# Kernel optimization log

Measured on AMD Instinct MI355X. Metric: run time of the kernel, lower is better.

The kernel has to match this reference:

```python
import jax, jax.numpy as jnp
import numpy as np

MARGIN = 0.09
SCALE_POS = 2.0
SCALE_NEG = 40.0
EPS = 1e-05
THRESH1 = 0.501
THRESH2 = 0.531


def setup_inputs() -> dict:
    key = jax.random.key(0)
    k1, k2 = jax.random.split(key)
    B, D, N_CLASSES = 4096, 1024, 64
    feats = jax.random.normal(k1, (B, D), dtype=jnp.float32)
    # thresholds in the loss assume cosine-scale similarities -> L2 normalize
    feats = feats / jnp.linalg.norm(feats, axis=1, keepdims=True)
    labels = jax.random.randint(k2, (B,), 0, N_CLASSES, dtype=jnp.int64)
    return {"feats": feats, "labels": labels}


def reference(feats, labels):
    B = feats.shape[0]
    sim = jnp.matmul(feats, feats.T)  # [B, B]
    eq = labels[:, None] == labels[None, :]
    neg_mask = ~eq
    pos_mask = eq & (sim < 1.0 - EPS)  # drops self-similarity (~1)
    # per-row max over negatives; rows with no negatives -> -inf -> no pos survive
    max_neg = jnp.max(jnp.where(neg_mask, sim, -jnp.inf), axis=1)  # [B]
    pos_mask = pos_mask & ((sim - MARGIN) < max_neg[:, None])
    n_pos = jnp.sum(pos_mask, axis=1)
    n_neg = jnp.sum(neg_mask, axis=1)
    pos_sum = jnp.sum(jnp.where(pos_mask, jnp.exp(-SCALE_POS * sim), 0.0), axis=1)
    neg_sum = jnp.sum(jnp.where(neg_mask, jnp.exp(SCALE_NEG * sim), 0.0), axis=1)
    pos_loss = (1.0 / SCALE_POS) * jnp.log(
        (pos_sum + np.exp(-SCALE_POS * THRESH1)) / (n_pos + 1.0))
    neg_loss = (1.0 / SCALE_NEG) * jnp.log(
        (neg_sum + np.exp(SCALE_NEG * THRESH2)) / (n_neg + 1.0))
    per_row = jnp.log(5.33 + jnp.exp(pos_loss + neg_loss))  # [B]
    valid = (n_neg >= 1) & (n_pos >= 1)
    return jnp.sum(jnp.where(valid, per_row, 0.0)) / B
```

## Files before the change

### kernel.cpp

```cpp
#include <hip/hip_runtime.h>
#include <hip/hip_bf16.h>
#include <math.h>

typedef __attribute__((ext_vector_type(8))) short short8;
typedef __attribute__((ext_vector_type(4))) float floatx4;

#define MARGIN_C   0.09f
#define SCALE_POS_C 2.0f
#define SCALE_NEG_C 40.0f
#define EPS_C      1e-5f
#define THRESH1_C  0.501f
#define THRESH2_C  0.531f

__device__ __forceinline__ unsigned short f2bf(float f) {
    unsigned u = __float_as_uint(f);
    u += 0x7fffu + ((u >> 16) & 1u);
    return (unsigned short)(u >> 16);
}

__device__ __forceinline__ void gld16(const void* g, void* l) {
    __builtin_amdgcn_global_load_lds(
        (const __attribute__((address_space(1))) void*)g,
        (__attribute__((address_space(3))) void*)l, 16, 0, 0);
}

__global__ __launch_bounds__(256) void cvt_bf16(const float* __restrict__ in,
                                                unsigned short* __restrict__ out,
                                                int n4) {
    int i = blockIdx.x * 256 + threadIdx.x;
    if (i >= n4) return;
    float4 v = ((const float4*)in)[i];
    ushort4 o;
    o.x = f2bf(v.x); o.y = f2bf(v.y); o.z = f2bf(v.z); o.w = f2bf(v.w);
    ((ushort4*)out)[i] = o;
}

__global__ __launch_bounds__(256) void gemm_sim(const unsigned short* __restrict__ fb,
                                                unsigned short* __restrict__ sim,
                                                int Bn, int Dn) {
    __shared__ __align__(16) unsigned short As[4096];
    __shared__ __align__(16) unsigned short Bs[4096];

    const int bid = blockIdx.x;
    int by = (int)((sqrtf(8.f * (float)bid + 1.f) - 1.f) * 0.5f);
    while ((by + 1) * (by + 2) / 2 <= bid) by++;
    while (by * (by + 1) / 2 > bid) by--;
    const int bx = bid - by * (by + 1) / 2;

    const int t    = threadIdx.x;
    const int wave = t >> 6;
    const int lane = t & 63;
    const int wr   = wave >> 1, wc = wave & 1;
    const int quad = lane >> 4, m16 = lane & 15;

    const int slot = t & 3;
    const int r0   = t >> 2;
    const int kf   = (slot + r0) & 3;
    const unsigned short* gA0 = fb + (size_t)(by * 128 + r0) * Dn + kf * 8;
    const unsigned short* gB0 = fb + (size_t)(bx * 128 + r0) * Dn + kf * 8;
    const unsigned short* gA1 = gA0 + (size_t)64 * Dn;
    const unsigned short* gB1 = gB0 + (size_t)64 * Dn;
    unsigned short* lA0 = As + t * 8;
    unsigned short* lA1 = As + 2048 + t * 8;
    unsigned short* lB0 = Bs + t * 8;
    unsigned short* lB1 = Bs + 2048 + t * 8;

    floatx4 acc[4][4];
#pragma unroll
    for (int i = 0; i < 4; i++)
#pragma unroll
        for (int j = 0; j < 4; j++) acc[i][j] = (floatx4){0.f, 0.f, 0.f, 0.f};

    const unsigned short* pa = As + (wr * 64 + m16) * 32 + ((quad - m16) & 3) * 8;
    const unsigned short* pb = Bs + (wc * 64 + m16) * 32 + ((quad - m16) & 3) * 8;

    for (int k0 = 0; k0 < Dn; k0 += 32) {
        gld16(gA0 + k0, lA0);
        gld16(gA1 + k0, lA1);
        gld16(gB0 + k0, lB0);
        gld16(gB1 + k0, lB1);
        __syncthreads();
        short8 af[4], bfr[4];
#pragma unroll
        for (int i = 0; i < 4; i++) af[i]  = *(const short8*)(pa + i * 512);
#pragma unroll
        for (int i = 0; i < 4; i++) bfr[i] = *(const short8*)(pb + i * 512);
#pragma unroll
        for (int i = 0; i < 4; i++)
#pragma unroll
            for (int j = 0; j < 4; j++)
                acc[i][j] = __builtin_amdgcn_mfma_f32_16x16x32_bf16(af[i], bfr[j], acc[i][j], 0, 0, 0);
        __syncthreads();
    }

    const int colBase = bx * 128 + wc * 64 + m16;
    const int rowBase = by * 128 + wr * 64 + quad * 4;
    const bool diag = (bx == by);
#pragma unroll
    for (int i = 0; i < 4; i++) {
#pragma unroll
        for (int j = 0; j < 4; j++) {
            const int col = colBase + j * 16;
            const int rb  = rowBase + i * 16;
#pragma unroll
            for (int r = 0; r < 4; r++) {
                const unsigned short v = f2bf(acc[i][j][r]);
                sim[(size_t)(rb + r) * Bn + col] = v;
                if (!diag) sim[(size_t)col * Bn + (rb + r)] = v;
            }
        }
    }
}

__global__ __launch_bounds__(256) void row_loss(const unsigned short* __restrict__ sim,
                                                const int* __restrict__ labels,
                                                float* __restrict__ per_row, int Bn) {
    __shared__ float red[20];
    const int t = threadIdx.x;
    const int row = blockIdx.x;
    const int wave = t >> 6, lane = t & 63;

    const int mylab = labels[row];

    const unsigned short* srow = sim + (size_t)row * Bn;
    float s[16];
    {
        const uint4* p = (const uint4*)srow + t * 2;
        uint4 v0 = p[0], v1 = p[1];
        unsigned w[8] = {v0.x, v0.y, v0.z, v0.w, v1.x, v1.y, v1.z, v1.w};
#pragma unroll
        for (int i = 0; i < 8; i++) {
            s[2 * i]     = __uint_as_float(w[i] << 16);
            s[2 * i + 1] = __uint_as_float(w[i] & 0xffff0000u);
        }
    }
    int lj[16];
    {
        const int4* lp = (const int4*)labels + t * 4;
        int4 a = lp[0], b = lp[1], c = lp[2], d = lp[3];
        lj[0]=a.x; lj[1]=a.y; lj[2]=a.z; lj[3]=a.w;
        lj[4]=b.x; lj[5]=b.y; lj[6]=b.z; lj[7]=b.w;
        lj[8]=c.x; lj[9]=c.y; lj[10]=c.z; lj[11]=c.w;
        lj[12]=d.x; lj[13]=d.y; lj[14]=d.z; lj[15]=d.w;
    }

    unsigned eqm = 0;
    float maxneg = -INFINITY, negsum = 0.f;
    int nneg = 0;
#pragma unroll
    for (int i = 0; i < 16; i++) {
        if (lj[i] == mylab) {
            eqm |= (1u << i);
        } else {
            nneg++;
            negsum += __expf(SCALE_NEG_C * s[i]);
            maxneg = fmaxf(maxneg, s[i]);
        }
    }

    float m = maxneg;
#pragma unroll
    for (int o = 32; o; o >>= 1) m = fmaxf(m, __shfl_down(m, o, 64));
    if (lane == 0) red[wave] = m;
    __syncthreads();
    maxneg = fmaxf(fmaxf(red[0], red[1]), fmaxf(red[2], red[3]));

    float possum = 0.f;
    int npos = 0;
#pragma unroll
    for (int i = 0; i < 16; i++) {
        if ((eqm >> i) & 1u) {
            float si = s[i];
            if (si < (1.0f - EPS_C) && (si - MARGIN_C) < maxneg) {
                npos++;
                possum += __expf(-SCALE_POS_C * si);
            }
        }
    }

    float a = negsum, b = possum, c = (float)nneg, d = (float)npos;
#pragma unroll
    for (int o = 32; o; o >>= 1) {
        a += __shfl_down(a, o, 64);
        b += __shfl_down(b, o, 64);
        c += __shfl_down(c, o, 64);
        d += __shfl_down(d, o, 64);
    }
    if (lane == 0) {
        red[4 + wave] = a; red[8 + wave] = b; red[12 + wave] = c; red[16 + wave] = d;
    }
    __syncthreads();
    if (t == 0) {
        float NS = red[4] + red[5] + red[6] + red[7];
        float PS = red[8] + red[9] + red[10] + red[11];
        float NN = red[12] + red[13] + red[14] + red[15];
        float NP = red[16] + red[17] + red[18] + red[19];
        float pr = 0.0f;
        if (NN >= 1.f && NP >= 1.f) {
            float pl = (1.f / SCALE_POS_C) * logf((PS + expf(-SCALE_POS_C * THRESH1_C)) / (NP + 1.f));
            float nl = (1.f / SCALE_NEG_C) * logf((NS + expf(SCALE_NEG_C * THRESH2_C)) / (NN + 1.f));
            pr = logf(5.33f + expf(pl + nl));
        }
        per_row[row] = pr;
    }
}

__global__ __launch_bounds__(256) void reduce_loss(const float* __restrict__ per_row,
                                                   float* __restrict__ out, int Bn) {
    __shared__ float red[4];
    const int t = threadIdx.x;
    const int wave = t >> 6, lane = t & 63;
    float acc = 0.f;
    const float4* p = (const float4*)per_row;
    for (int i = t; i < Bn / 4; i += 256) {
        float4 v = p[i];
        acc += (v.x + v.y) + (v.z + v.w);
    }
#pragma unroll
    for (int o = 32; o; o >>= 1) acc += __shfl_down(acc, o, 64);
    if (lane == 0) red[wave] = acc;
    __syncthreads();
    if (t == 0) out[0] = (red[0] + red[1] + red[2] + red[3]) / (float)Bn;
}

extern "C" void kernel_launch(void* const* d_in, const int* in_sizes, int n_in,
                              void* d_out, int out_size, void* d_ws, size_t ws_size,
                              hipStream_t stream) {
    const float* feats = (const float*)d_in[0];
    const int* labels  = (const int*)d_in[1];
    float* out = (float*)d_out;

    const int Bn = in_sizes[1];
    const int Dn = in_sizes[0] / Bn;

    unsigned short* fb  = (unsigned short*)d_ws;
    unsigned short* sim = fb + (size_t)Bn * Dn;
    float* per_row = (float*)(sim + (size_t)Bn * Bn);

    const int n4 = (Bn * Dn) / 4;
    cvt_bf16<<<(n4 + 255) / 256, 256, 0, stream>>>(feats, fb, n4);

    const int nt = Bn / 128;
    const int ntri = nt * (nt + 1) / 2;
    gemm_sim<<<ntri, 256, 0, stream>>>(fb, sim, Bn, Dn);

    row_loss<<<Bn, 256, 0, stream>>>(sim, labels, per_row, Bn);
    reduce_loss<<<1, 256, 0, stream>>>(per_row, out, Bn);
}
```

Before: 134.1 us.

## Fuse negative stats into GEMM epilogue and compute positives per class

Result: slower. 150.0 us (+11.9%).

```diff
diff --git a/kernel.cpp b/kernel.cpp
--- a/kernel.cpp
+++ b/kernel.cpp
@@ -5,29 +5,30 @@
 typedef __attribute__((ext_vector_type(8))) short short8;
 typedef __attribute__((ext_vector_type(4))) float floatx4;
 
-#define MARGIN_C   0.09f
-#define SCALE_POS_C 2.0f
-#define SCALE_NEG_C 40.0f
-#define EPS_C      1e-5f
-#define THRESH1_C  0.501f
-#define THRESH2_C  0.531f
+#define MARGIN_C    0.09f
+#define ONE_M_EPS   0.99999f
+#define NCLS        64
+#define MEMSTRIDE   256
 
 __device__ __forceinline__ unsigned short f2bf(float f) {
     unsigned u = __float_as_uint(f);
     u += 0x7fffu + ((u >> 16) & 1u);
     return (unsigned short)(u >> 16);
 }
-
-__device__ __forceinline__ void gld16(const void* g, void* l) {
-    __builtin_amdgcn_global_load_lds(
-        (const __attribute__((address_space(1))) void*)g,
-        (__attribute__((address_space(3))) void*)l, 16, 0, 0);
+__device__ __forceinline__ unsigned fkey(float f) {
+    unsigned u = __float_as_uint(f);
+    return (u >> 31) ? ~u : (u | 0x80000000u);
+}
+__device__ __forceinline__ float fdec(unsigned k) {
+    return __uint_as_float((k >> 31) ? (k & 0x7fffffffu) : ~k);
 }
 
 __global__ __launch_bounds__(256) void cvt_bf16(const float* __restrict__ in,
                                                 unsigned short* __restrict__ out,
-                                                int n4) {
+                                                float* __restrict__ statz,
+                                                int n4, int nz4) {
     int i = blockIdx.x * 256 + threadIdx.x;
+    if (i < nz4) ((float4*)statz)[i] = make_float4(0.f, 0.f, 0.f, 0.f);
     if (i >= n4) return;
     float4 v = ((const float4*)in)[i];
     ushort4 o;
@@ -35,11 +36,31 @@
     ((ushort4*)out)[i] = o;
 }
 
-__global__ __launch_bounds__(256) void gemm_sim(const unsigned short* __restrict__ fb,
-                                                unsigned short* __restrict__ sim,
-                                                int Bn, int Dn) {
-    __shared__ __align__(16) unsigned short As[4096];
-    __shared__ __align__(16) unsigned short Bs[4096];
+__global__ __launch_bounds__(256) void build_members(const int* __restrict__ labels,
+                                                     int* __restrict__ members,
+                                                     int* __restrict__ classCount, int Bn) {
+    __shared__ int cnt;
+    const int c = blockIdx.x;
+    if (threadIdx.x == 0) cnt = 0;
+    __syncthreads();
+    for (int j = threadIdx.x; j < Bn; j += 256) {
+        if (labels[j] == c) {
+            int p = atomicAdd(&cnt, 1);
+            if (p < MEMSTRIDE) members[c * MEMSTRIDE + p] = j;
+        }
+    }
+    __syncthreads();
+    if (threadIdx.x == 0) classCount[c] = (cnt < MEMSTRIDE) ? cnt : MEMSTRIDE;
+}
+
+__global__ __launch_bounds__(256) void gemm_fused(const unsigned short* __restrict__ fb,
+                                                  const int* __restrict__ labels,
+                                                  float* __restrict__ negsum,
+                                                  unsigned* __restrict__ negmax,
+                                                  int Bn, int Dn) {
+    __shared__ __align__(16) unsigned short As[2][4096];
+    __shared__ __align__(16) unsigned short Bs[2][4096];
+    __shared__ int Lrow[128], Lcol[128];
 
     const int bid = blockIdx.x;
     int by = (int)((sqrtf(8.f * (float)bid + 1.f) - 1.f) * 0.5f);
@@ -47,23 +68,19 @@
     while (by * (by + 1) / 2 > bid) by--;
     const int bx = bid - by * (by + 1) / 2;
 
-    const int t    = threadIdx.x;
-    const int wave = t >> 6;
-    const int lane = t & 63;
-    const int wr   = wave >> 1, wc = wave & 1;
+    const int t = threadIdx.x;
+    const int wave = t >> 6, lane = t & 63;
+    const int wr = wave >> 1, wc = wave & 1;
     const int quad = lane >> 4, m16 = lane & 15;
 
-    const int slot = t & 3;
-    const int r0   = t >> 2;
-    const int kf   = (slot + r0) & 3;
-    const unsigned short* gA0 = fb + (size_t)(by * 128 + r0) * Dn + kf * 8;
-    const unsigned short* gB0 = fb + (size_t)(bx * 128 + r0) * Dn + kf * 8;
+    if (t < 128) Lrow[t] = labels[by * 128 + t];
+    else         Lcol[t - 128] = labels[bx * 128 + (t - 128)];
+
+    const int lr = t >> 2, slot = t & 3, kf = (slot + lr) & 3;
+    const unsigned short* gA0 = fb + (size_t)(by * 128 + lr) * Dn + kf * 8;
+    const unsigned short* gB0 = fb + (size_t)(bx * 128 + lr) * Dn + kf * 8;
     const unsigned short* gA1 = gA0 + (size_t)64 * Dn;
     const unsigned short* gB1 = gB0 + (size_t)64 * Dn;
-    unsigned short* lA0 = As + t * 8;
-    unsigned short* lA1 = As + 2048 + t * 8;
-    unsigned short* lB0 = Bs + t * 8;
-    unsigned short* lB1 = Bs + 2048 + t * 8;
 
     floatx4 acc[4][4];
 #pragma unroll
@@ -71,156 +88,245 @@
 #pragma unroll
         for (int j = 0; j < 4; j++) acc[i][j] = (floatx4){0.f, 0.f, 0.f, 0.f};
 
-    const unsigned short* pa = As + (wr * 64 + m16) * 32 + ((quad - m16) & 3) * 8;
-    const unsigned short* pb = Bs + (wc * 64 + m16) * 32 + ((quad - m16) & 3) * 8;
-
-    for (int k0 = 0; k0 < Dn; k0 += 32) {
-        gld16(gA0 + k0, lA0);
-        gld16(gA1 + k0, lA1);
-        gld16(gB0 + k0, lB0);
-        gld16(gB1 + k0, lB1);
-        __syncthreads();
+    const int fragA = (wr * 64 + m16) * 32 + ((quad - m16) & 3) * 8;
+    const int fragB = (wc * 64 + m16) * 32 + ((quad - m16) & 3) * 8;
+
+    const int NS = Dn / 32;
+    uint4 ra0 = *(const uint4*)gA0, ra1 = *(const uint4*)gA1;
+    uint4 rb0 = *(const uint4*)gB0, rb1 = *(const uint4*)gB1;
+    *(uint4*)(&As[0][t * 8]) = ra0;  *(uint4*)(&As[0][2048 + t * 8]) = ra1;
+    *(uint4*)(&Bs[0][t * 8]) = rb0;  *(uint4*)(&Bs[0][2048 + t * 8]) = rb1;
+    ra0 = *(const uint4*)(gA0 + 32); ra1 = *(const uint4*)(gA1 + 32);
+    rb0 = *(const uint4*)(gB0 + 32); rb1 = *(const uint4*)(gB1 + 32);
+    __syncthreads();
+
+    for (int s = 0; s < NS; s++) {
+        const unsigned short* as_ = As[s & 1];
+        const unsigned short* bs_ = Bs[s & 1];
         short8 af[4], bfr[4];
 #pragma unroll
-        for (int i = 0; i < 4; i++) af[i]  = *(const short8*)(pa + i * 512);
-#pragma unroll
-        for (int i = 0; i < 4; i++) bfr[i] = *(const short8*)(pb + i * 512);
+        for (int i = 0; i < 4; i++) af[i]  = *(const short8*)(as_ + fragA + i * 512);
+#pragma unroll
+        for (int i = 0; i < 4; i++) bfr[i] = *(const short8*)(bs_ + fragB + i * 512);
 #pragma unroll
         for (int i = 0; i < 4; i++)
 #pragma unroll
             for (int j = 0; j < 4; j++)
                 acc[i][j] = __builtin_amdgcn_mfma_f32_16x16x32_bf16(af[i], bfr[j], acc[i][j], 0, 0, 0);
-        __syncthreads();
-    }
-
-    const int colBase = bx * 128 + wc * 64 + m16;
-    const int rowBase = by * 128 + wr * 64 + quad * 4;
-    const bool diag = (bx == by);
+        if (s + 1 < NS) {
+            __syncthreads();
+            unsigned short* aw = As[(s + 1) & 1];
+            unsigned short* bw = Bs[(s + 1) & 1];
+            *(uint4*)(&aw[t * 8]) = ra0;  *(uint4*)(&aw[2048 + t * 8]) = ra1;
+            *(uint4*)(&bw[t * 8]) = rb0;  *(uint4*)(&bw[2048 + t * 8]) = rb1;
+            if (s + 2 < NS) {
+                const int ko = (s + 2) * 32;
+                ra0 = *(const uint4*)(gA0 + ko); ra1 = *(const uint4*)(gA1 + ko);
+                rb0 = *(const uint4*)(gB0 + ko); rb1 = *(const uint4*)(gB1 + ko);
+            }
+            __syncthreads();
+        }
+    }
+
+    int cl[4];
+#pragma unroll
+    for (int j = 0; j < 4; j++) cl[j] = Lcol[wc * 64 + j * 16 + m16];
+
+    float nsm[4] = {0.f, 0.f, 0.f, 0.f};
+    float nmm[4] = {-INFINITY, -INFINITY, -INFINITY, -INFINITY};
+
 #pragma unroll
     for (int i = 0; i < 4; i++) {
 #pragma unroll
+        for (int r = 0; r < 4; r++) {
+            const int rowl = wr * 64 + i * 16 + quad * 4 + r;
+            const int rl = Lrow[rowl];
+            float ns = 0.f, nm = -INFINITY;
+#pragma unroll
+            for (int j = 0; j < 4; j++) {
+                float s = acc[i][j][r];
+                if (cl[j] != rl) {
+                    float e = __expf(40.f * s);
+                    ns += e;
+                    nm = fmaxf(nm, s);
+                    nsm[j] += e;
+                    nmm[j] = fmaxf(nmm[j], s);
+                }
+            }
+#pragma unroll
+            for (int o = 8; o; o >>= 1) {
+                ns += __shfl_down(ns, o, 64);
+                nm = fmaxf(nm, __shfl_down(nm, o, 64));
+            }
+            if (m16 == 0) {
+                const int gr = by * 128 + rowl;
+                atomicAdd(negsum + gr, ns);
+                atomicMax(negmax + gr, fkey(nm));
+            }
+        }
+    }
+    if (bx != by) {
+#pragma unroll
         for (int j = 0; j < 4; j++) {
-            const int col = colBase + j * 16;
-            const int rb  = rowBase + i * 16;
-#pragma unroll
-            for (int r = 0; r < 4; r++) {
-                const unsigned short v = f2bf(acc[i][j][r]);
-                sim[(size_t)(rb + r) * Bn + col] = v;
-                if (!diag) sim[(size_t)col * Bn + (rb + r)] = v;
-            }
-        }
-    }
-}
-
-__global__ __launch_bounds__(256) void row_loss(const unsigned short* __restrict__ sim,
-                                                const int* __restrict__ labels,
-                                                float* __restrict__ per_row, int Bn) {
-    __shared__ float red[20];
+            float v = nsm[j], m = nmm[j];
+            v += __shfl_down(v, 16, 64);
+            m = fmaxf(m, __shfl_down(m, 16, 64));
+            v += __shfl_down(v, 32, 64);
+            m = fmaxf(m, __shfl_down(m, 32, 64));
+            if (quad == 0) {
+                const int gc = bx * 128 + wc * 64 + j * 16 + m16;
+                atomicAdd(negsum + gc, v);
+                atomicMax(negmax + gc, fkey(m));
+            }
+        }
+    }
+}
+
+__global__ __launch_bounds__(256) void pos_class(const unsigned short* __restrict__ fb,
+                                                 const int* __restrict__ members,
+                                                 const int* __restrict__ classCount,
+                                                 const unsigned* __restrict__ negmax,
+                                                 float* __restrict__ possum,
+                                                 float* __restrict__ nposf,
+                                                 int Bn, int Dn) {
+    __shared__ __align__(16) unsigned short As[2][4096];
+    __shared__ __align__(16) unsigned short Bs[2][4096];
+
+    const int c = blockIdx.x;
+    const int n = classCount[c];
+    if (n <= 0) return;
+    const int base = c * MEMSTRIDE;
+    const int m0 = members[base];
+
     const int t = threadIdx.x;
-    const int row = blockIdx.x;
     const int wave = t >> 6, lane = t & 63;
-
-    const int mylab = labels[row];
-
-    const unsigned short* srow = sim + (size_t)row * Bn;
-    float s[16];
-    {
-        const uint4* p = (const uint4*)srow + t * 2;
-        uint4 v0 = p[0], v1 = p[1];
-        unsigned w[8] = {v0.x, v0.y, v0.z, v0.w, v1.x, v1.y, v1.z, v1.w};
-#pragma unroll
-        for (int i = 0; i < 8; i++) {
-            s[2 * i]     = __uint_as_float(w[i] << 16);
-            s[2 * i + 1] = __uint_as_float(w[i] & 0xffff0000u);
-        }
-    }
-    int lj[16];
-    {
-        const int4* lp = (const int4*)labels + t * 4;
-        int4 a = lp[0], b = lp[1], c = lp[2], d = lp[3];
-        lj[0]=a.x; lj[1]=a.y; lj[2]=a.z; lj[3]=a.w;
-        lj[4]=b.x; lj[5]=b.y; lj[6]=b.z; lj[7]=b.w;
-        lj[8]=c.x; lj[9]=c.y; lj[10]=c.z; lj[11]=c.w;
-        lj[12]=d.x; lj[13]=d.y; lj[14]=d.z; lj[15]=d.w;
-    }
-
-    unsigned eqm = 0;
-    float maxneg = -INFINITY, negsum = 0.f;
-    int nneg = 0;
-#pragma unroll
-    for (int i = 0; i < 16; i++) {
-        if (lj[i] == mylab) {
-            eqm |= (1u << i);
-        } else {
-            nneg++;
-            negsum += __expf(SCALE_NEG_C * s[i]);
-            maxneg = fmaxf(maxneg, s[i]);
-        }
-    }
-
-    float m = maxneg;
-#pragma unroll
-    for (int o = 32; o; o >>= 1) m = fmaxf(m, __shfl_down(m, o, 64));
-    if (lane == 0) red[wave] = m;
-    __syncthreads();
-    maxneg = fmaxf(fmaxf(red[0], red[1]), fmaxf(red[2], red[3]));
-
-    float possum = 0.f;
-    int npos = 0;
-#pragma unroll
-    for (int i = 0; i < 16; i++) {
-        if ((eqm >> i) & 1u) {
-            float si = s[i];
-            if (si < (1.0f - EPS_C) && (si - MARGIN_C) < maxneg) {
-                npos++;
-                possum += __expf(-SCALE_POS_C * si);
-            }
-        }
-    }
-
-    float a = negsum, b = possum, c = (float)nneg, d = (float)npos;
-#pragma unroll
-    for (int o = 32; o; o >>= 1) {
-        a += __shfl_down(a, o, 64);
-        b += __shfl_down(b, o, 64);
-        c += __shfl_down(c, o, 64);
-        d += __shfl_down(d, o, 64);
-    }
-    if (lane == 0) {
-        red[4 + wave] = a; red[8 + wave] = b; red[12 + wave] = c; red[16 + wave] = d;
-    }
-    __syncthreads();
-    if (t == 0) {
-        float NS = red[4] + red[5] + red[6] + red[7];
-        float PS = red[8] + red[9] + red[10] + red[11];
-        float NN = red[12] + red[13] + red[14] + red[15];
-        float NP = red[16] + red[17] + red[18] + red[19];
-        float pr = 0.0f;
-        if (NN >= 1.f && NP >= 1.f) {
-            float pl = (1.f / SCALE_POS_C) * logf((PS + expf(-SCALE_POS_C * THRESH1_C)) / (NP + 1.f));
-            float nl = (1.f / SCALE_NEG_C) * logf((NS + expf(SCALE_NEG_C * THRESH2_C)) / (NN + 1.f));
-            pr = logf(5.33f + expf(pl + nl));
-        }
-        per_row[row] = pr;
-    }
-}
-
-__global__ __launch_bounds__(256) void reduce_loss(const float* __restrict__ per_row,
-                                                   float* __restrict__ out, int Bn) {
-    __shared__ float red[4];
+    const int wr = wave >> 1, wc = wave & 1;
+    const int quad = lane >> 4, m16 = lane & 15;
+
+    const int lr = t >> 2, slot = t & 3, kf = (slot + lr) & 3;
+    const int fragA = (wr * 64 + m16) * 32 + ((quad - m16) & 3) * 8;
+    const int fragB = (wc * 64 + m16) * 32 + ((quad - m16) & 3) * 8;
+    const int NS = Dn / 32;
+
+    for (int r0 = 0; r0 < n; r0 += 128) {
+        for (int c0 = 0; c0 < n; c0 += 128) {
+            __syncthreads();
+            const int i0 = r0 + lr, i1 = r0 + lr + 64;
+            const int j0 = c0 + lr, j1 = c0 + lr + 64;
+            const int a0i = (i0 < n) ? members[base + i0] : m0;
+            const int a1i = (i1 < n) ? members[base + i1] : m0;
+            const int b0i = (j0 < n) ? members[base + j0] : m0;
+            const int b1i = (j1 < n) ? members[base + j1] : m0;
+            const unsigned short* gA0 = fb + (size_t)a0i * Dn + kf * 8;
+            const unsigned short* gA1 = fb + (size_t)a1i * Dn + kf * 8;
+            const unsigned short* gB0 = fb + (size_t)b0i * Dn + kf * 8;
+            const unsigned short* gB1 = fb + (size_t)b1i * Dn + kf * 8;
+
+            floatx4 acc[4][4];
+#pragma unroll
+            for (int i = 0; i < 4; i++)
+#pragma unroll
+                for (int j = 0; j < 4; j++) acc[i][j] = (floatx4){0.f, 0.f, 0.f, 0.f};
+
+            uint4 ra0 = *(const uint4*)gA0, ra1 = *(const uint4*)gA1;
+            uint4 rb0 = *(const uint4*)gB0, rb1 = *(const uint4*)gB1;
+            *(uint4*)(&As[0][t * 8]) = ra0;  *(uint4*)(&As[0][2048 + t * 8]) = ra1;
+            *(uint4*)(&Bs[0][t * 8]) = rb0;  *(uint4*)(&Bs[0][2048 + t * 8]) = rb1;
+            ra0 = *(const uint4*)(gA0 + 32); ra1 = *(const uint4*)(gA1 + 32);
+            rb0 = *(const uint4*)(gB0 + 32); rb1 = *(const uint4*)(gB1 + 32);
+            __syncthreads();
+
+            for (int s = 0; s < NS; s++) {
+                const unsigned short* as_ = As[s & 1];
+                const unsigned short* bs_ = Bs[s & 1];
+                short8 af[4], bfr[4];
+#pragma unroll
+                for (int i = 0; i < 4; i++) af[i]  = *(const short8*)(as_ + fragA + i * 512);
+#pragma unroll
+                for (int i = 0; i < 4; i++) bfr[i] = *(const short8*)(bs_ + fragB + i * 512);
+#pragma unroll
+                for (int i = 0; i < 4; i++)
+#pragma unroll
+                    for (int j = 0; j < 4; j++)
+                        acc[i][j] = __builtin_amdgcn_mfma_f32_16x16x32_bf16(af[i], bfr[j], acc[i][j], 0, 0, 0);
+                if (s + 1 < NS) {
+                    __syncthreads();
+                    unsigned short* aw = As[(s + 1) & 1];
+                    unsigned short* bw = Bs[(s + 1) & 1];
+                    *(uint4*)(&aw[t * 8]) = ra0;  *(uint4*)(&aw[2048 + t * 8]) = ra1;
+                    *(uint4*)(&bw[t * 8]) = rb0;  *(uint4*)(&bw[2048 + t * 8]) = rb1;
+                    if (s + 2 < NS) {
+                        const int ko = (s + 2) * 32;
+                        ra0 = *(const uint4*)(gA0 + ko); ra1 = *(const uint4*)(gA1 + ko);
+                        rb0 = *(const uint4*)(gB0 + ko); rb1 = *(const uint4*)(gB1 + ko);
+                    }
+                    __syncthreads();
+                }
+            }
+
+#pragma unroll
+            for (int i = 0; i < 4; i++) {
+#pragma unroll
+                for (int r = 0; r < 4; r++) {
+                    const int rowl = wr * 64 + i * 16 + quad * 4 + r;
+                    const int idx = r0 + rowl;
+                    const bool vr = idx < n;
+                    const int gi = vr ? members[base + idx] : 0;
+                    const float mx = vr ? fdec(negmax[gi]) : -1e30f;
+                    float pp = 0.f, pc = 0.f;
+#pragma unroll
+                    for (int j = 0; j < 4; j++) {
+                        const int cj = c0 + wc * 64 + j * 16 + m16;
+                        float s = acc[i][j][r];
+                        if (vr && cj < n && s < ONE_M_EPS && (s - MARGIN_C) < mx) {
+                            pp += __expf(-2.f * s);
+                            pc += 1.f;
+                        }
+                    }
+#pragma unroll
+                    for (int o = 8; o; o >>= 1) {
+                        pp += __shfl_down(pp, o, 64);
+                        pc += __shfl_down(pc, o, 64);
+                    }
+                    if (m16 == 0 && vr) {
+                        atomicAdd(possum + gi, pp);
+                        atomicAdd(nposf + gi, pc);
+                    }
+                }
+            }
+        }
+    }
+}
+
+__global__ __launch_bounds__(1024) void finalize(const float* __restrict__ negsum,
+                                                 const float* __restrict__ possum,
+                                                 const float* __restrict__ nposf,
+                                                 const int* __restrict__ labels,
+                                                 const int* __restrict__ classCount,
+                                                 float* __restrict__ out, int Bn) {
+    __shared__ float red[16];
     const int t = threadIdx.x;
     const int wave = t >> 6, lane = t & 63;
     float acc = 0.f;
-    const float4* p = (const float4*)per_row;
-    for (int i = t; i < Bn / 4; i += 256) {
-        float4 v = p[i];
-        acc += (v.x + v.y) + (v.z + v.w);
+    for (int i = t; i < Bn; i += 1024) {
+        const int lab = labels[i];
+        const int nneg = Bn - classCount[lab];
+        const float np = nposf[i];
+        if (nneg >= 1 && np >= 0.5f) {
+            float pl = 0.5f * logf((possum[i] + expf(-2.f * 0.501f)) / (np + 1.f));
+            float nl = (1.f / 40.f) * logf((negsum[i] + expf(40.f * 0.531f)) / ((float)nneg + 1.f));
+            acc += logf(5.33f + expf(pl + nl));
+        }
     }
 #pragma unroll
     for (int o = 32; o; o >>= 1) acc += __shfl_down(acc, o, 64);
     if (lane == 0) red[wave] = acc;
     __syncthreads();
-    if (t == 0) out[0] = (red[0] + red[1] + red[2] + red[3]) / (float)Bn;
+    if (t == 0) {
+        float s = 0.f;
+        for (int w = 0; w < 16; w++) s += red[w];
+        out[0] = s / (float)Bn;
+    }
 }
 
 extern "C" void kernel_launch(void* const* d_in, const int* in_sizes, int n_in,
@@ -233,17 +339,25 @@
     const int Bn = in_sizes[1];
     const int Dn = in_sizes[0] / Bn;
 
-    unsigned short* fb  = (unsigned short*)d_ws;
-    unsigned short* sim = fb + (size_t)Bn * Dn;
-    float* per_row = (float*)(sim + (size_t)Bn * Bn);
+    unsigned short* fb = (unsigned short*)d_ws;
+    float* stats   = (float*)(fb + (size_t)Bn * Dn);
+    float* negsum  = stats;
+    unsigned* negmax = (unsigned*)(stats + Bn);
+    float* possum  = stats + 2 * Bn;
+    float* nposf   = stats + 3 * Bn;
+    int* classCount = (int*)(stats + 4 * Bn);
+    int* members    = classCount + NCLS;
 
     const int n4 = (Bn * Dn) / 4;
-    cvt_bf16<<<(n4 + 255) / 256, 256, 0, stream>>>(feats, fb, n4);
+    cvt_bf16<<<(n4 + 255) / 256, 256, 0, stream>>>(feats, fb, stats, n4, Bn);
+
+    build_members<<<NCLS, 256, 0, stream>>>(labels, members, classCount, Bn);
 
     const int nt = Bn / 128;
     const int ntri = nt * (nt + 1) / 2;
-    gemm_sim<<<ntri, 256, 0, stream>>>(fb, sim, Bn, Dn);
-
-    row_loss<<<Bn, 256, 0, stream>>>(sim, labels, per_row, Bn);
-    reduce_loss<<<1, 256, 0, stream>>>(per_row, out, Bn);
-}
+    gemm_fused<<<ntri, 256, 0, stream>>>(fb, labels, negsum, negmax, Bn, Dn);
+
+    pos_class<<<NCLS, 256, 0, stream>>>(fb, members, classCount, negmax, possum, nposf, Bn, Dn);
+
+    finalize<<<1, 1024, 0, stream>>>(negsum, possum, nposf, labels, classCount, out, Bn);
+}
```
